# Kernel optimization log

Hardware: AMD Instinct MI355X
Metric: run time of the kernel (lower is better)

## Reference

```python
import jax, jax.numpy as jnp
import numpy as np


def _rms_norm(x, eps=1e-5):
    x32 = x.astype(jnp.float32)
    var = jnp.mean(x32 * x32, axis=-1, keepdims=True)
    return (x32 * jax.lax.rsqrt(var + eps)).astype(x.dtype)


def _rotate_half(x):
    x1, x2 = jnp.split(x, 2, axis=-1)
    return jnp.concatenate([-x2, x1], axis=-1)


def setup_inputs() -> dict:
    key = jax.random.key(0)
    ks = jax.random.split(key, 8)
    B, N, d, dh = 1, 4096, 1024, 64
    inner, k = 2816, 3
    # realistic RoPE cache [N, dh]
    pos = jnp.arange(N, dtype=jnp.float32)[:, None]
    inv = 1.0 / (10000.0 ** (jnp.arange(0, dh, 2, dtype=jnp.float32) / dh))
    ang = pos * inv[None, :]
    ang = jnp.concatenate([ang, ang], axis=-1)
    return {
        'Q_in': jax.random.normal(ks[0], (B, N, d), jnp.float32),
        'cos': jnp.cos(ang),
        'sin': jnp.sin(ang),
        'W_qkv': jax.random.normal(ks[1], (d, 3 * d), jnp.float32) * 0.02,
        'W_o': jax.random.normal(ks[2], (d, d), jnp.float32) * 0.02,
        'W_up': jax.random.normal(ks[3], (d, 2 * inner), jnp.float32) * 0.02,
        'conv_w': jax.random.normal(ks[4], (k, 1, inner), jnp.float32) * 0.1,
        'conv_b': jax.random.normal(ks[5], (inner,), jnp.float32) * 0.01,
        'W_down': jax.random.normal(ks[6], (inner, d), jnp.float32) * 0.02,
    }


def reference(Q_in, cos, sin, W_qkv, W_o, W_up, conv_w, conv_b, W_down):
    B, N, d = Q_in.shape
    H = 16
    dh = d // H
    qkv = (Q_in @ W_qkv).reshape(B, N, 3, H, dh)
    Qp, Kp, Vp = qkv[:, :, 0], qkv[:, :, 1], qkv[:, :, 2]
    # RoPE: cos/sin [N, dh] broadcast over batch and heads
    cb = cos[None, :, None, :]
    sb = sin[None, :, None, :]
    Qp = Qp * cb + _rotate_half(Qp) * sb
    Kp = Kp * cb + _rotate_half(Kp) * sb
    Q = _rms_norm(jnp.transpose(Qp, (0, 2, 1, 3)))  # [B,H,N,dh]
    K = _rms_norm(jnp.transpose(Kp, (0, 2, 1, 3)))
    V = jnp.transpose(Vp, (0, 2, 1, 3))
    # (elu+1)^2 positive-kernel attention (full N x N matrix, as in the source)
    S = jnp.einsum('bhnd,bhmd->bhnm', Q, K) * (dh ** -0.5)
    W = jax.nn.elu(S) + 1.0
    W = W * W  # kernel_power == 2
    Attr = jnp.einsum('bhnm,bhmd->bhnd', W, V)
    C = Attr / (jnp.sum(W, axis=-1, keepdims=True) + 1e-6)
    m = C - V
    m_concat = jnp.transpose(m, (0, 2, 1, 3)).reshape(B, N, d)
    Q_interact = _rms_norm(Q_in + m_concat @ W_o)
    # ConvSwiGLU FFN
    GU = Q_interact @ W_up
    G, U = jnp.split(GU, 2, axis=-1)
    Hf = jax.nn.silu(G) * U  # [B,N,inner]
    Hc = jax.lax.conv_general_dilated(
        Hf, conv_w, window_strides=(1,), padding=[(1, 1)],
        dimension_numbers=('NWC', 'WIO', 'NWC'),
        feature_group_count=Hf.shape[-1])
    Hc = jax.nn.silu(Hc + conv_b)
    return _rms_norm(Q_interact + Hc @ W_down)
```

## Files before the change

### kernel.cpp

```cpp
#include <hip/hip_runtime.h>
#include <hip/hip_bf16.h>
#include <cstdint>

#define N_TOK   4096
#define D_MODEL 1024
#define N_HEAD  16
#define DH      64
#define INNER   2816

typedef __attribute__((ext_vector_type(8))) short bf16x8;
typedef __attribute__((ext_vector_type(4))) float f32x4;
typedef __attribute__((ext_vector_type(8))) unsigned short us8v;
typedef __attribute__((ext_vector_type(4))) unsigned short us4v;

union BF16x8U { bf16x8 v; uint32_t u[4]; };

__device__ __forceinline__ unsigned short f2bf(float x) {
    union { __hip_bfloat16 h; unsigned short u; } c;
    c.h = __float2bfloat16(x);
    return c.u;
}

__device__ __forceinline__ float bf2f(unsigned short u) {
    union { float f; uint32_t i; } c;
    c.i = ((uint32_t)u) << 16;
    return c.f;
}

__device__ __forceinline__ float silu_f(float x) {
    return x / (1.f + __expf(-x));
}

__global__ __launch_bounds__(256) void cvt_bf16(
    const float* __restrict__ in, unsigned short* __restrict__ out) {
    const size_t i8 = ((size_t)blockIdx.x * 256 + threadIdx.x) * 8;
    float4 a = *reinterpret_cast<const float4*>(&in[i8]);
    float4 b = *reinterpret_cast<const float4*>(&in[i8 + 4]);
    us8v o;
    o[0] = f2bf(a.x); o[1] = f2bf(a.y); o[2] = f2bf(a.z); o[3] = f2bf(a.w);
    o[4] = f2bf(b.x); o[5] = f2bf(b.y); o[6] = f2bf(b.z); o[7] = f2bf(b.w);
    *reinterpret_cast<us8v*>(&out[i8]) = o;
}

__global__ __launch_bounds__(256) void transpose_bf16(
    const float* __restrict__ W, unsigned short* __restrict__ WT,
    int K, int N) {
    __shared__ unsigned short T[64][65];
    const int n0 = blockIdx.x * 64;
    const int k0 = blockIdx.y * 64;
    const int t = threadIdx.x;
#pragma unroll
    for (int i = 0; i < 4; ++i) {
        const int id = i * 256 + t;
        const int r = id >> 4;
        const int c = (id & 15) * 4;
        float4 v = *reinterpret_cast<const float4*>(
            &W[(size_t)(k0 + r) * N + n0 + c]);
        T[c + 0][r] = f2bf(v.x);
        T[c + 1][r] = f2bf(v.y);
        T[c + 2][r] = f2bf(v.z);
        T[c + 3][r] = f2bf(v.w);
    }
    __syncthreads();
#pragma unroll
    for (int i = 0; i < 2; ++i) {
        const int id = i * 256 + t;
        const int n = id >> 3;
        const int c = (id & 7) * 8;
        us8v o;
#pragma unroll
        for (int j = 0; j < 8; ++j) o[j] = T[n][c + j];
        *reinterpret_cast<us8v*>(&WT[(size_t)(n0 + n) * K + k0 + c]) = o;
    }
}

template<int OBF>
__global__ __launch_bounds__(256) void gemm_bf16(
    const unsigned short* __restrict__ A, const unsigned short* __restrict__ Bt,
    void* __restrict__ Cout, int M, int N, int K) {
    __shared__ unsigned short As[128 * 72];
    __shared__ unsigned short Bs[128 * 72];
    const int tid = threadIdx.x;
    const int lane = tid & 63;
    const int w = tid >> 6;
    const int l15 = lane & 15, lg = lane >> 4;
    const int wm = w >> 1, wn = w & 1;
    const int rowBase = blockIdx.y * 128;
    const int colBase = blockIdx.x * 128;

    f32x4 acc[4][4];
#pragma unroll
    for (int i = 0; i < 4; ++i)
#pragma unroll
        for (int j = 0; j < 4; ++j) acc[i][j] = (f32x4){0.f, 0.f, 0.f, 0.f};

    for (int k0 = 0; k0 < K; k0 += 64) {
        us8v a_r[4], b_r[4];
#pragma unroll
        for (int i = 0; i < 4; ++i) {
            const int ch = i * 256 + tid;
            const int r = ch >> 3, c = (ch & 7) * 8;
            a_r[i] = *reinterpret_cast<const us8v*>(
                &A[(size_t)(rowBase + r) * K + k0 + c]);
            b_r[i] = *reinterpret_cast<const us8v*>(
                &Bt[(size_t)(colBase + r) * K + k0 + c]);
        }
        __syncthreads();
#pragma unroll
        for (int i = 0; i < 4; ++i) {
            const int ch = i * 256 + tid;
            const int r = ch >> 3, c = (ch & 7) * 8;
            *reinterpret_cast<us8v*>(&As[r * 72 + c]) = a_r[i];
            *reinterpret_cast<us8v*>(&Bs[r * 72 + c]) = b_r[i];
        }
        __syncthreads();
        bf16x8 af[2][4], bfr[2][4];
#pragma unroll
        for (int kk = 0; kk < 2; ++kk) {
#pragma unroll
            for (int f = 0; f < 4; ++f) {
                af[kk][f] = *reinterpret_cast<const bf16x8*>(
                    &As[(wm * 64 + f * 16 + l15) * 72 + kk * 32 + lg * 8]);
                bfr[kk][f] = *reinterpret_cast<const bf16x8*>(
                    &Bs[(wn * 64 + f * 16 + l15) * 72 + kk * 32 + lg * 8]);
            }
        }
#pragma unroll
        for (int kk = 0; kk < 2; ++kk)
#pragma unroll
            for (int mf = 0; mf < 4; ++mf)
#pragma unroll
                for (int nf = 0; nf < 4; ++nf)
                    acc[mf][nf] = __builtin_amdgcn_mfma_f32_16x16x32_bf16(
                        bfr[kk][nf], af[kk][mf], acc[mf][nf], 0, 0, 0);
    }
#pragma unroll
    for (int mf = 0; mf < 4; ++mf) {
#pragma unroll
        for (int nf = 0; nf < 4; ++nf) {
            const size_t m = rowBase + wm * 64 + mf * 16 + l15;
            const size_t n = colBase + wn * 64 + nf * 16 + lg * 4;
            if (OBF) {
                us4v o;
                o[0] = f2bf(acc[mf][nf][0]); o[1] = f2bf(acc[mf][nf][1]);
                o[2] = f2bf(acc[mf][nf][2]); o[3] = f2bf(acc[mf][nf][3]);
                *reinterpret_cast<us4v*>(
                    &((unsigned short*)Cout)[m * N + n]) = o;
            } else {
                float4 o;
                o.x = acc[mf][nf][0]; o.y = acc[mf][nf][1];
                o.z = acc[mf][nf][2]; o.w = acc[mf][nf][3];
                *reinterpret_cast<float4*>(&((float*)Cout)[m * N + n]) = o;
            }
        }
    }
}

__global__ __launch_bounds__(256) void rope_norm2(
    const float* __restrict__ qkv, const float* __restrict__ cosb,
    const float* __restrict__ sinb, unsigned short* __restrict__ Qb,
    unsigned short* __restrict__ Kb, unsigned short* __restrict__ Vt,
    unsigned short* __restrict__ Vb) {
    const int h = blockIdx.y;
    const int n0 = blockIdx.x * 64;
    const int wv = threadIdx.x >> 6;
    const int lane = threadIdx.x & 63;
    __shared__ unsigned short Vs[64][66];
#pragma unroll 1
    for (int it = 0; it < 16; ++it) {
        const int tn = it * 4 + wv;
        const int n = n0 + tn;
        const float* base = qkv + (size_t)n * (3 * D_MODEL) + h * DH;
        float qv = base[lane];
        float kv = base[D_MODEL + lane];
        float vv = base[2 * D_MODEL + lane];
        const float c = cosb[n * DH + lane];
        const float s = sinb[n * DH + lane];
        const float qp = __shfl(qv, lane ^ 32, 64);
        const float kp = __shfl(kv, lane ^ 32, 64);
        const float sgn = (lane < 32) ? -1.f : 1.f;
        qv = qv * c + sgn * qp * s;
        kv = kv * c + sgn * kp * s;
        float sq = qv * qv, sk = kv * kv;
#pragma unroll
        for (int off = 32; off > 0; off >>= 1) {
            sq += __shfl_xor(sq, off, 64);
            sk += __shfl_xor(sk, off, 64);
        }
        qv *= rsqrtf(sq * (1.f / DH) + 1e-5f);
        kv *= rsqrtf(sk * (1.f / DH) + 1e-5f);
        const size_t o = ((size_t)h * N_TOK + n) * DH + lane;
        Qb[o] = f2bf(qv);
        Kb[o] = f2bf(kv);
        Vb[o] = f2bf(vv);
        Vs[tn][lane] = f2bf(vv);
    }
    __syncthreads();
    const int d = threadIdx.x >> 2;
    const int c0 = (threadIdx.x & 3) * 16;
    us8v o0, o1;
#pragma unroll
    for (int i = 0; i < 8; ++i) o0[i] = Vs[c0 + i][d];
#pragma unroll
    for (int i = 0; i < 8; ++i) o1[i] = Vs[c0 + 8 + i][d];
    unsigned short* dst = Vt + ((size_t)h * DH + d) * N_TOK + n0 + c0;
    *reinterpret_cast<us8v*>(dst) = o0;
    *reinterpret_cast<us8v*>(dst + 8) = o1;
}

__global__ __launch_bounds__(256, 2) void attn_mfma2(
    const unsigned short* __restrict__ Qb, const unsigned short* __restrict__ Kb,
    const unsigned short* __restrict__ Vt, const unsigned short* __restrict__ Vb,
    unsigned short* __restrict__ Mout) {
    const int B = blockIdx.x;
    const int h = ((B & 7) << 1) | ((B >> 3) & 1);
    const int q0 = (B >> 4) * 64;
    const int lane = threadIdx.x & 63;
    const int wv = threadIdx.x >> 6;
    const int l15 = lane & 15, lg = lane >> 4;
    const unsigned short* Qh = Qb + (size_t)h * N_TOK * DH;
    const unsigned short* Kh = Kb + (size_t)h * N_TOK * DH;
    const unsigned short* Vth = Vt + (size_t)h * DH * N_TOK;

    bf16x8 qf[4][2];
#pragma unroll
    for (int qs = 0; qs < 4; ++qs) {
        const unsigned short* qp = Qh + (size_t)(q0 + qs * 16 + l15) * DH + lg * 8;
        qf[qs][0] = *reinterpret_cast<const bf16x8*>(qp);
        qf[qs][1] = *reinterpret_cast<const bf16x8*>(qp + 32);
    }

    f32x4 ct[4][4];
#pragma unroll
    for (int i = 0; i < 4; ++i)
#pragma unroll
        for (int j = 0; j < 4; ++j) ct[i][j] = (f32x4){0.f, 0.f, 0.f, 0.f};
    float dpart[4] = {0.f, 0.f, 0.f, 0.f};

    const int sA = l15 + ((lg & 1) << 5);
    const int sB = sA + 16;
    const bool hi = (lg & 2) != 0;

#pragma unroll 1
    for (int kt = 0; kt < 16; ++kt) {
        const int k0 = (wv * 16 + kt) * 64;
        const unsigned short* kp = Kh + (size_t)(k0 + l15) * DH + lg * 8;
        bf16x8 kf[4][2];
#pragma unroll
        for (int ks = 0; ks < 4; ++ks) {
            kf[ks][0] = *reinterpret_cast<const bf16x8*>(kp + ks * 16 * DH);
            kf[ks][1] = *reinterpret_cast<const bf16x8*>(kp + ks * 16 * DH + 32);
        }
        const unsigned short* vp = Vth + (size_t)l15 * N_TOK + k0 + lg * 8;
        bf16x8 vf[4][2];
#pragma unroll
        for (int ds = 0; ds < 4; ++ds) {
            vf[ds][0] = *reinterpret_cast<const bf16x8*>(vp + (size_t)ds * 16 * N_TOK);
            vf[ds][1] = *reinterpret_cast<const bf16x8*>(vp + (size_t)ds * 16 * N_TOK + 32);
        }
#pragma unroll
        for (int qs = 0; qs < 4; ++qs) {
            f32x4 st[4];
#pragma unroll
            for (int ks = 0; ks < 4; ++ks) {
                f32x4 z = (f32x4){0.f, 0.f, 0.f, 0.f};
                z = __builtin_amdgcn_mfma_f32_16x16x32_bf16(kf[ks][0], qf[qs][0], z, 0, 0, 0);
                st[ks] = __builtin_amdgcn_mfma_f32_16x16x32_bf16(kf[ks][1], qf[qs][1], z, 0, 0, 0);
            }
            uint32_t wpk[4][2];
#pragma unroll
            for (int ks = 0; ks < 4; ++ks) {
                float w4[4];
#pragma unroll
                for (int r = 0; r < 4; ++r) {
                    const float x = st[ks][r] * 0.125f;
                    float e = fmaxf(x, 0.f) + __expf(fminf(x, 0.f));
                    e = e * e;
                    w4[r] = e;
                    dpart[qs] += e;
                }
                wpk[ks][0] = (uint32_t)f2bf(w4[0]) | ((uint32_t)f2bf(w4[1]) << 16);
                wpk[ks][1] = (uint32_t)f2bf(w4[2]) | ((uint32_t)f2bf(w4[3]) << 16);
            }
#pragma unroll
            for (int kh = 0; kh < 2; ++kh) {
                const uint32_t a0 = (uint32_t)__shfl((int)wpk[2 * kh][0], sA, 64);
                const uint32_t a1 = (uint32_t)__shfl((int)wpk[2 * kh][1], sA, 64);
                const uint32_t a2 = (uint32_t)__shfl((int)wpk[2 * kh][0], sB, 64);
                const uint32_t a3 = (uint32_t)__shfl((int)wpk[2 * kh][1], sB, 64);
                const uint32_t b0 = (uint32_t)__shfl((int)wpk[2 * kh + 1][0], sA, 64);
                const uint32_t b1 = (uint32_t)__shfl((int)wpk[2 * kh + 1][1], sA, 64);
                const uint32_t b2 = (uint32_t)__shfl((int)wpk[2 * kh + 1][0], sB, 64);
                const uint32_t b3 = (uint32_t)__shfl((int)wpk[2 * kh + 1][1], sB, 64);
                BF16x8U bb;
                bb.u[0] = hi ? b0 : a0;
                bb.u[1] = hi ? b1 : a1;
                bb.u[2] = hi ? b2 : a2;
                bb.u[3] = hi ? b3 : a3;
#pragma unroll
                for (int ds = 0; ds < 4; ++ds)
                    ct[qs][ds] = __builtin_amdgcn_mfma_f32_16x16x32_bf16(
                        vf[ds][kh], bb.v, ct[qs][ds], 0, 0, 0);
            }
        }
    }

    __shared__ float accs[4][64][72];
    __shared__ float dens[4][64];
#pragma unroll
    for (int qs = 0; qs < 4; ++qs) {
        const int q = qs * 16 + l15;
#pragma unroll
        for (int ds = 0; ds < 4; ++ds) {
            *reinterpret_cast<f32x4*>(&accs[wv][q][ds * 16 + lg * 4]) = ct[qs][ds];
        }
        float dp = dpart[qs];
        dp += __shfl_xor(dp, 16, 64);
        dp += __shfl_xor(dp, 32, 64);
        if (lg == 0) dens[wv][q] = dp;
    }
    __syncthreads();
    const int q = threadIdx.x >> 2;
    const int dbase = (threadIdx.x & 3) * 16;
    const float dn = 1.f / (dens[0][q] + dens[1][q] + dens[2][q] + dens[3][q] + 1e-6f);
    const unsigned short* Vh = Vb + ((size_t)h * N_TOK + (q0 + q)) * DH;
    unsigned short* Mrow = Mout + (size_t)(q0 + q) * D_MODEL + h * DH;
#pragma unroll
    for (int t = 0; t < 4; ++t) {
        const int d = dbase + t * 4;
        f32x4 s0 = *reinterpret_cast<const f32x4*>(&accs[0][q][d]);
        f32x4 s1 = *reinterpret_cast<const f32x4*>(&accs[1][q][d]);
        f32x4 s2 = *reinterpret_cast<const f32x4*>(&accs[2][q][d]);
        f32x4 s3 = *reinterpret_cast<const f32x4*>(&accs[3][q][d]);
        const us4v vv = *reinterpret_cast<const us4v*>(&Vh[d]);
        us4v o;
#pragma unroll
        for (int r = 0; r < 4; ++r) {
            const float a = s0[r] + s1[r] + s2[r] + s3[r];
            o[r] = f2bf(a * dn - bf2f(vv[r]));
        }
        *reinterpret_cast<us4v*>(&Mrow[d]) = o;
    }
}

template<int WB>
__global__ __launch_bounds__(256) void rms_resid2(
    const float* __restrict__ X, const float* __restrict__ R,
    float* __restrict__ O32, unsigned short* __restrict__ Obf) {
    const int row = blockIdx.x;
    const int tid = threadIdx.x;
    const float4 xv = reinterpret_cast<const float4*>(X + (size_t)row * D_MODEL)[tid];
    const float4 rv = reinterpret_cast<const float4*>(R + (size_t)row * D_MODEL)[tid];
    const float t0 = xv.x + rv.x, t1 = xv.y + rv.y, t2 = xv.z + rv.z, t3 = xv.w + rv.w;
    float ss = t0 * t0 + t1 * t1 + t2 * t2 + t3 * t3;
#pragma unroll
    for (int off = 32; off > 0; off >>= 1) ss += __shfl_xor(ss, off, 64);
    __shared__ float red[4];
    if ((tid & 63) == 0) red[tid >> 6] = ss;
    __syncthreads();
    const float tot = red[0] + red[1] + red[2] + red[3];
    const float rs = rsqrtf(tot * (1.f / D_MODEL) + 1e-5f);
    float4 o;
    o.x = t0 * rs; o.y = t1 * rs; o.z = t2 * rs; o.w = t3 * rs;
    reinterpret_cast<float4*>(O32 + (size_t)row * D_MODEL)[tid] = o;
    if (WB) {
        us4v ob;
        ob[0] = f2bf(o.x); ob[1] = f2bf(o.y); ob[2] = f2bf(o.z); ob[3] = f2bf(o.w);
        *reinterpret_cast<us4v*>(&Obf[(size_t)row * D_MODEL + tid * 4]) = ob;
    }
}

__global__ __launch_bounds__(256) void silu_mul_bf(
    const unsigned short* __restrict__ GU, unsigned short* __restrict__ Hf) {
    const size_t idx = (size_t)blockIdx.x * 256 + threadIdx.x;
    const int c8 = (int)(idx % (INNER / 8)) * 8;
    const int n = (int)(idx / (INNER / 8));
    us8v g = *reinterpret_cast<const us8v*>(&GU[(size_t)n * (2 * INNER) + c8]);
    us8v u = *reinterpret_cast<const us8v*>(&GU[(size_t)n * (2 * INNER) + INNER + c8]);
    us8v o;
#pragma unroll
    for (int j = 0; j < 8; ++j) {
        const float gv = bf2f(g[j]);
        o[j] = f2bf(silu_f(gv) * bf2f(u[j]));
    }
    *reinterpret_cast<us8v*>(&Hf[(size_t)n * INNER + c8]) = o;
}

__global__ __launch_bounds__(256) void dwconv_bf(
    const unsigned short* __restrict__ Hf, const float* __restrict__ W,
    const float* __restrict__ Bv, unsigned short* __restrict__ Hc) {
    const size_t idx = (size_t)blockIdx.x * 256 + threadIdx.x;
    const int c8 = (int)(idx % (INNER / 8)) * 8;
    const int n = (int)(idx / (INNER / 8));
    float a[8];
    {
        float4 b0 = *reinterpret_cast<const float4*>(&Bv[c8]);
        float4 b1 = *reinterpret_cast<const float4*>(&Bv[c8 + 4]);
        a[0] = b0.x; a[1] = b0.y; a[2] = b0.z; a[3] = b0.w;
        a[4] = b1.x; a[5] = b1.y; a[6] = b1.z; a[7] = b1.w;
    }
#pragma unroll
    for (int k = 0; k < 3; ++k) {
        const int nn = n + k - 1;
        if (nn >= 0 && nn < N_TOK) {
            us8v x = *reinterpret_cast<const us8v*>(&Hf[(size_t)nn * INNER + c8]);
            float4 w0 = *reinterpret_cast<const float4*>(&W[(size_t)k * INNER + c8]);
            float4 w1 = *reinterpret_cast<const float4*>(&W[(size_t)k * INNER + c8 + 4]);
            a[0] += bf2f(x[0]) * w0.x; a[1] += bf2f(x[1]) * w0.y;
            a[2] += bf2f(x[2]) * w0.z; a[3] += bf2f(x[3]) * w0.w;
            a[4] += bf2f(x[4]) * w1.x; a[5] += bf2f(x[5]) * w1.y;
            a[6] += bf2f(x[6]) * w1.z; a[7] += bf2f(x[7]) * w1.w;
        }
    }
    us8v o;
#pragma unroll
    for (int j = 0; j < 8; ++j) o[j] = f2bf(silu_f(a[j]));
    *reinterpret_cast<us8v*>(&Hc[(size_t)n * INNER + c8]) = o;
}

extern "C" void kernel_launch(void* const* d_in, const int* in_sizes, int n_in,
                              void* d_out, int out_size, void* d_ws, size_t ws_size,
                              hipStream_t stream) {
    const float* Qin   = (const float*)d_in[0];
    const float* cosb  = (const float*)d_in[1];
    const float* sinb  = (const float*)d_in[2];
    const float* Wqkv  = (const float*)d_in[3];
    const float* Wo    = (const float*)d_in[4];
    const float* Wup   = (const float*)d_in[5];
    const float* convw = (const float*)d_in[6];
    const float* convb = (const float*)d_in[7];
    const float* Wdown = (const float*)d_in[8];
    float* out = (float*)d_out;
    float* ws  = (float*)d_ws;

    unsigned short* WqkvT  = (unsigned short*)(ws);
    unsigned short* WoT    = (unsigned short*)(ws + 1572864);
    unsigned short* WupT   = (unsigned short*)(ws + 2097152);
    unsigned short* WdownT = (unsigned short*)(ws + 4980736);
    unsigned short* Qin_bf = (unsigned short*)(ws + 6422528);
    unsigned short* mcat   = (unsigned short*)(ws + 6422528);
    float*          qkv32  = ws + 8519680;
    float*          wo32   = ws + 8519680;
    unsigned short* GU     = (unsigned short*)(ws + 8519680);
    unsigned short* Hc     = (unsigned short*)(ws + 8519680);
    float*          dn32   = ws + 14286848;
    unsigned short* Qb     = (unsigned short*)(ws + 21102592);
    unsigned short* Kb     = (unsigned short*)(ws + 23199744);
    unsigned short* Vt     = (unsigned short*)(ws + 25296896);
    unsigned short* Vb     = (unsigned short*)(ws + 27394048);
    unsigned short* Hf     = (unsigned short*)(ws + 21102592);
    float*          Qi32   = ws + 29491200;
    unsigned short* Qi_bf  = (unsigned short*)(ws + 33685504);

    const dim3 blk(256);
    cvt_bf16<<<2048, blk, 0, stream>>>(Qin, Qin_bf);
    transpose_bf16<<<dim3(48, 16), blk, 0, stream>>>(Wqkv, WqkvT, 1024, 3072);
    transpose_bf16<<<dim3(16, 16), blk, 0, stream>>>(Wo, WoT, 1024, 1024);
    transpose_bf16<<<dim3(88, 16), blk, 0, stream>>>(Wup, WupT, 1024, 5632);
    transpose_bf16<<<dim3(16, 44), blk, 0, stream>>>(Wdown, WdownT, 2816, 1024);
    gemm_bf16<0><<<dim3(24, 32), blk, 0, stream>>>(
        Qin_bf, WqkvT, qkv32, 4096, 3072, 1024);
    rope_norm2<<<dim3(64, 16), blk, 0, stream>>>(qkv32, cosb, sinb, Qb, Kb, Vt, Vb);
    attn_mfma2<<<1024, blk, 0, stream>>>(Qb, Kb, Vt, Vb, mcat);
    gemm_bf16<0><<<dim3(8, 32), blk, 0, stream>>>(
        mcat, WoT, wo32, 4096, 1024, 1024);
    rms_resid2<1><<<4096, blk, 0, stream>>>(wo32, Qin, Qi32, Qi_bf);
    gemm_bf16<1><<<dim3(44, 32), blk, 0, stream>>>(
        Qi_bf, WupT, GU, 4096, 5632, 1024);
    silu_mul_bf<<<5632, blk, 0, stream>>>(GU, Hf);
    dwconv_bf<<<5632, blk, 0, stream>>>(Hf, convw, convb, Hc);
    gemm_bf16<0><<<dim3(8, 32), blk, 0, stream>>>(
        Hc, WdownT, dn32, 4096, 1024, 2816);
    rms_resid2<0><<<4096, blk, 0, stream>>>(dn32, Qi32, out, nullptr);
}
```

Measured before the change: 461.1 us.

## Use direct global-to-LDS loads in GEMM and slim attention epilogue

```diff
diff --git a/kernel.cpp b/kernel.cpp
--- a/kernel.cpp
+++ b/kernel.cpp
@@ -29,6 +29,12 @@
 
 __device__ __forceinline__ float silu_f(float x) {
     return x / (1.f + __expf(-x));
+}
+
+__device__ __forceinline__ void gld16(const unsigned short* g, unsigned short* l) {
+    __builtin_amdgcn_global_load_lds(
+        (const __attribute__((address_space(1))) void*)g,
+        (__attribute__((address_space(3))) void*)l, 16, 0, 0);
 }
 
 __global__ __launch_bounds__(256) void cvt_bf16(
@@ -78,8 +84,8 @@
 __global__ __launch_bounds__(256) void gemm_bf16(
     const unsigned short* __restrict__ A, const unsigned short* __restrict__ Bt,
     void* __restrict__ Cout, int M, int N, int K) {
-    __shared__ unsigned short As[128 * 72];
-    __shared__ unsigned short Bs[128 * 72];
+    __shared__ unsigned short As[128 * 64];
+    __shared__ unsigned short Bs[128 * 64];
     const int tid = threadIdx.x;
     const int lane = tid & 63;
     const int w = tid >> 6;
@@ -88,6 +94,11 @@
     const int rowBase = blockIdx.y * 128;
     const int colBase = blockIdx.x * 128;
 
+    const int srow = w * 32 + (lane >> 3);
+    const int scol = (lane & 7) * 8;
+    const unsigned short* Ag = &A[(size_t)(rowBase + srow) * K + scol];
+    const unsigned short* Bg = &Bt[(size_t)(colBase + srow) * K + scol];
+
     f32x4 acc[4][4];
 #pragma unroll
     for (int i = 0; i < 4; ++i)
@@ -95,23 +106,10 @@
         for (int j = 0; j < 4; ++j) acc[i][j] = (f32x4){0.f, 0.f, 0.f, 0.f};
 
     for (int k0 = 0; k0 < K; k0 += 64) {
-        us8v a_r[4], b_r[4];
-#pragma unroll
-        for (int i = 0; i < 4; ++i) {
-            const int ch = i * 256 + tid;
-            const int r = ch >> 3, c = (ch & 7) * 8;
-            a_r[i] = *reinterpret_cast<const us8v*>(
-                &A[(size_t)(rowBase + r) * K + k0 + c]);
-            b_r[i] = *reinterpret_cast<const us8v*>(
-                &Bt[(size_t)(colBase + r) * K + k0 + c]);
-        }
-        __syncthreads();
-#pragma unroll
-        for (int i = 0; i < 4; ++i) {
-            const int ch = i * 256 + tid;
-            const int r = ch >> 3, c = (ch & 7) * 8;
-            *reinterpret_cast<us8v*>(&As[r * 72 + c]) = a_r[i];
-            *reinterpret_cast<us8v*>(&Bs[r * 72 + c]) = b_r[i];
+#pragma unroll
+        for (int j = 0; j < 4; ++j) {
+            gld16(Ag + (size_t)j * 8 * K + k0, &As[(w * 32 + j * 8) * 64]);
+            gld16(Bg + (size_t)j * 8 * K + k0, &Bs[(w * 32 + j * 8) * 64]);
         }
         __syncthreads();
         bf16x8 af[2][4], bfr[2][4];
@@ -120,9 +118,9 @@
 #pragma unroll
             for (int f = 0; f < 4; ++f) {
                 af[kk][f] = *reinterpret_cast<const bf16x8*>(
-                    &As[(wm * 64 + f * 16 + l15) * 72 + kk * 32 + lg * 8]);
+                    &As[(wm * 64 + f * 16 + l15) * 64 + kk * 32 + lg * 8]);
                 bfr[kk][f] = *reinterpret_cast<const bf16x8*>(
-                    &Bs[(wn * 64 + f * 16 + l15) * 72 + kk * 32 + lg * 8]);
+                    &Bs[(wn * 64 + f * 16 + l15) * 64 + kk * 32 + lg * 8]);
             }
         }
 #pragma unroll
@@ -133,6 +131,7 @@
                 for (int nf = 0; nf < 4; ++nf)
                     acc[mf][nf] = __builtin_amdgcn_mfma_f32_16x16x32_bf16(
                         bfr[kk][nf], af[kk][mf], acc[mf][nf], 0, 0, 0);
+        __syncthreads();
     }
 #pragma unroll
     for (int mf = 0; mf < 4; ++mf) {
@@ -187,7 +186,7 @@
             sq += __shfl_xor(sq, off, 64);
             sk += __shfl_xor(sk, off, 64);
         }
-        qv *= rsqrtf(sq * (1.f / DH) + 1e-5f);
+        qv *= rsqrtf(sq * (1.f / DH) + 1e-5f) * 0.125f;
         kv *= rsqrtf(sk * (1.f / DH) + 1e-5f);
         const size_t o = ((size_t)h * N_TOK + n) * DH + lane;
         Qb[o] = f2bf(qv);
@@ -208,7 +207,7 @@
     *reinterpret_cast<us8v*>(dst + 8) = o1;
 }
 
-__global__ __launch_bounds__(256, 2) void attn_mfma2(
+__global__ __launch_bounds__(256, 4) void attn_mfma2(
     const unsigned short* __restrict__ Qb, const unsigned short* __restrict__ Kb,
     const unsigned short* __restrict__ Vt, const unsigned short* __restrict__ Vb,
     unsigned short* __restrict__ Mout) {
@@ -261,19 +260,21 @@
 #pragma unroll
         for (int qs = 0; qs < 4; ++qs) {
             f32x4 st[4];
+            __builtin_amdgcn_s_setprio(1);
 #pragma unroll
             for (int ks = 0; ks < 4; ++ks) {
                 f32x4 z = (f32x4){0.f, 0.f, 0.f, 0.f};
                 z = __builtin_amdgcn_mfma_f32_16x16x32_bf16(kf[ks][0], qf[qs][0], z, 0, 0, 0);
                 st[ks] = __builtin_amdgcn_mfma_f32_16x16x32_bf16(kf[ks][1], qf[qs][1], z, 0, 0, 0);
             }
+            __builtin_amdgcn_s_setprio(0);
             uint32_t wpk[4][2];
 #pragma unroll
             for (int ks = 0; ks < 4; ++ks) {
                 float w4[4];
 #pragma unroll
                 for (int r = 0; r < 4; ++r) {
-                    const float x = st[ks][r] * 0.125f;
+                    const float x = st[ks][r];
                     float e = fmaxf(x, 0.f) + __expf(fminf(x, 0.f));
                     e = e * e;
                     w4[r] = e;
@@ -297,49 +298,71 @@
                 bb.u[1] = hi ? b1 : a1;
                 bb.u[2] = hi ? b2 : a2;
                 bb.u[3] = hi ? b3 : a3;
+                __builtin_amdgcn_s_setprio(1);
 #pragma unroll
                 for (int ds = 0; ds < 4; ++ds)
                     ct[qs][ds] = __builtin_amdgcn_mfma_f32_16x16x32_bf16(
                         vf[ds][kh], bb.v, ct[qs][ds], 0, 0, 0);
-            }
-        }
-    }
-
-    __shared__ float accs[4][64][72];
+                __builtin_amdgcn_s_setprio(0);
+            }
+        }
+    }
+
+    __shared__ float accs2[2][64][72];
     __shared__ float dens[4][64];
 #pragma unroll
     for (int qs = 0; qs < 4; ++qs) {
-        const int q = qs * 16 + l15;
-#pragma unroll
-        for (int ds = 0; ds < 4; ++ds) {
-            *reinterpret_cast<f32x4*>(&accs[wv][q][ds * 16 + lg * 4]) = ct[qs][ds];
-        }
         float dp = dpart[qs];
         dp += __shfl_xor(dp, 16, 64);
         dp += __shfl_xor(dp, 32, 64);
-        if (lg == 0) dens[wv][q] = dp;
+        if (lg == 0) dens[wv][qs * 16 + l15] = dp;
+    }
+    if (wv >= 2) {
+#pragma unroll
+        for (int qs = 0; qs < 4; ++qs)
+#pragma unroll
+            for (int ds = 0; ds < 4; ++ds)
+                *reinterpret_cast<f32x4*>(
+                    &accs2[wv - 2][qs * 16 + l15][ds * 16 + lg * 4]) = ct[qs][ds];
     }
     __syncthreads();
-    const int q = threadIdx.x >> 2;
-    const int dbase = (threadIdx.x & 3) * 16;
-    const float dn = 1.f / (dens[0][q] + dens[1][q] + dens[2][q] + dens[3][q] + 1e-6f);
-    const unsigned short* Vh = Vb + ((size_t)h * N_TOK + (q0 + q)) * DH;
-    unsigned short* Mrow = Mout + (size_t)(q0 + q) * D_MODEL + h * DH;
-#pragma unroll
-    for (int t = 0; t < 4; ++t) {
-        const int d = dbase + t * 4;
-        f32x4 s0 = *reinterpret_cast<const f32x4*>(&accs[0][q][d]);
-        f32x4 s1 = *reinterpret_cast<const f32x4*>(&accs[1][q][d]);
-        f32x4 s2 = *reinterpret_cast<const f32x4*>(&accs[2][q][d]);
-        f32x4 s3 = *reinterpret_cast<const f32x4*>(&accs[3][q][d]);
-        const us4v vv = *reinterpret_cast<const us4v*>(&Vh[d]);
-        us4v o;
-#pragma unroll
-        for (int r = 0; r < 4; ++r) {
-            const float a = s0[r] + s1[r] + s2[r] + s3[r];
-            o[r] = f2bf(a * dn - bf2f(vv[r]));
-        }
-        *reinterpret_cast<us4v*>(&Mrow[d]) = o;
+    if (wv < 2) {
+#pragma unroll
+        for (int qs = 0; qs < 4; ++qs)
+#pragma unroll
+            for (int ds = 0; ds < 4; ++ds)
+                ct[qs][ds] += *reinterpret_cast<const f32x4*>(
+                    &accs2[wv][qs * 16 + l15][ds * 16 + lg * 4]);
+        if (wv == 1) {
+#pragma unroll
+            for (int qs = 0; qs < 4; ++qs)
+#pragma unroll
+                for (int ds = 0; ds < 4; ++ds)
+                    *reinterpret_cast<f32x4*>(
+                        &accs2[1][qs * 16 + l15][ds * 16 + lg * 4]) = ct[qs][ds];
+        }
+    }
+    __syncthreads();
+    if (wv == 0) {
+#pragma unroll
+        for (int qs = 0; qs < 4; ++qs) {
+            const int q = qs * 16 + l15;
+            const float dnq = 1.f /
+                (dens[0][q] + dens[1][q] + dens[2][q] + dens[3][q] + 1e-6f);
+            const unsigned short* Vrow = Vb + ((size_t)h * N_TOK + q0 + q) * DH;
+            unsigned short* Mrow = Mout + (size_t)(q0 + q) * D_MODEL + h * DH;
+#pragma unroll
+            for (int ds = 0; ds < 4; ++ds) {
+                const int d = ds * 16 + lg * 4;
+                const f32x4 s1 = *reinterpret_cast<const f32x4*>(&accs2[1][q][d]);
+                const us4v vv = *reinterpret_cast<const us4v*>(&Vrow[d]);
+                us4v o;
+#pragma unroll
+                for (int r = 0; r < 4; ++r)
+                    o[r] = f2bf((ct[qs][ds][r] + s1[r]) * dnq - bf2f(vv[r]));
+                *reinterpret_cast<us4v*>(&Mrow[d]) = o;
+            }
+        }
     }
 }
 
```

Result: slower. 1.026 ms (+122.5%).
